# Kernel tuning notes

Measured on AMD Instinct MI355X. Metric: run time of the kernel, lower is better.

## Reference

```python
import jax, jax.numpy as jnp
import numpy as np

B, S, D = 2, 2048, 1024
FC = 4096
H = 16
EPS = 1e-5


def _layer_norm(x, g, b):
    mu = jnp.mean(x, axis=-1, keepdims=True)
    var = jnp.var(x, axis=-1, keepdims=True)
    return (x - mu) * jax.lax.rsqrt(var + EPS) * g + b


def setup_inputs() -> dict:
    key = jax.random.key(0)
    ks = jax.random.split(key, 8)
    s = 0.02
    return {
        "x": jax.random.normal(ks[0], (B, S, D), dtype=jnp.float32),
        "ln1_g": jnp.ones((D,), jnp.float32),
        "ln1_b": jnp.zeros((D,), jnp.float32),
        "w_qkv": jax.random.normal(ks[1], (D, 3 * D), dtype=jnp.float32) * s,
        "b_qkv": jnp.zeros((3 * D,), jnp.float32),
        "ln2_g": jnp.ones((D,), jnp.float32),
        "ln2_b": jnp.zeros((D,), jnp.float32),
        "w1": jax.random.normal(ks[2], (D, FC), dtype=jnp.float32) * s,
        "b1": jnp.zeros((FC,), jnp.float32),
        "w2": jax.random.normal(ks[3], (FC, D), dtype=jnp.float32) * s,
        "b2": jnp.zeros((D,), jnp.float32),
    }


def reference(x, ln1_g, ln1_b, w_qkv, b_qkv, ln2_g, ln2_b, w1, b1, w2, b2):
    # pre-LN attention block
    h = _layer_norm(x, ln1_g, ln1_b)
    qkv = h @ w_qkv + b_qkv                       # [B,S,3D]
    q, k, v = jnp.split(qkv, 3, axis=-1)
    hd = D // H
    q = q.reshape(B, S, H, hd)
    k = k.reshape(B, S, H, hd)
    v = v.reshape(B, S, H, hd)
    scale = 1.0 / jnp.sqrt(jnp.float32(hd))
    scores = jnp.einsum("bqhd,bkhd->bhqk", q, k) * scale
    a = jax.nn.softmax(scores, axis=-1)           # [B,H,S,S]
    attn = jnp.einsum("bhqk,bkhd->bqhd", a, v).reshape(B, S, D)
    attn = attn + x
    # MLP block
    h2 = _layer_norm(attn, ln2_g, ln2_b)
    m = jax.nn.relu(h2 @ w1 + b1)
    out = m @ w2 + b2 + attn
    return out
```

## Files before the change

### kernel.cpp

```cpp
#include <hip/hip_runtime.h>
#include <stdint.h>

typedef __bf16 bf16x8 __attribute__((ext_vector_type(8)));
typedef __bf16 bf16x4 __attribute__((ext_vector_type(4)));
typedef float f32x4 __attribute__((ext_vector_type(4)));

__device__ __forceinline__ void g2l16(const void* gp, void* lp) {
  __builtin_amdgcn_global_load_lds(
      (__attribute__((address_space(1))) void*)const_cast<void*>(gp),
      (__attribute__((address_space(3))) void*)lp, 16, 0, 0);
}

__global__ __launch_bounds__(256) void ln_bf16(
    const float* __restrict__ in, const float* __restrict__ g,
    const float* __restrict__ b, __bf16* __restrict__ out) {
  int row = blockIdx.x;
  int t = threadIdx.x;
  const float4* rp = (const float4*)(in + (size_t)row * 1024);
  float4 v = rp[t];
  float s = v.x + v.y + v.z + v.w;
  float ss = v.x * v.x + v.y * v.y + v.z * v.z + v.w * v.w;
#pragma unroll
  for (int o = 32; o; o >>= 1) {
    s += __shfl_down(s, o, 64);
    ss += __shfl_down(ss, o, 64);
  }
  __shared__ float red[8];
  int w = t >> 6;
  if ((t & 63) == 0) { red[w] = s; red[4 + w] = ss; }
  __syncthreads();
  float S1 = red[0] + red[1] + red[2] + red[3];
  float S2 = red[4] + red[5] + red[6] + red[7];
  float mu = S1 * (1.0f / 1024.0f);
  float var = S2 * (1.0f / 1024.0f) - mu * mu;
  float rstd = rsqrtf(var + 1e-5f);
  int c = t * 4;
  float4 gv = ((const float4*)g)[t];
  float4 bv = ((const float4*)b)[t];
  __bf16* op = out + (size_t)row * 1024 + c;
  op[0] = (__bf16)((v.x - mu) * rstd * gv.x + bv.x);
  op[1] = (__bf16)((v.y - mu) * rstd * gv.y + bv.y);
  op[2] = (__bf16)((v.z - mu) * rstd * gv.z + bv.z);
  op[3] = (__bf16)((v.w - mu) * rstd * gv.w + bv.w);
}

__global__ __launch_bounds__(256) void tcast(const float* __restrict__ in,
                                             __bf16* __restrict__ out, int R,
                                             int C) {
  __shared__ float t[32][33];
  int c0 = blockIdx.x * 32, r0 = blockIdx.y * 32;
  int tx = threadIdx.x & 31, ty = threadIdx.x >> 5;
#pragma unroll
  for (int i = 0; i < 4; i++)
    t[ty + i * 8][tx] = in[(size_t)(r0 + ty + i * 8) * C + c0 + tx];
  __syncthreads();
#pragma unroll
  for (int i = 0; i < 4; i++)
    out[(size_t)(c0 + ty + i * 8) * R + r0 + tx] = (__bf16)t[tx][ty + i * 8];
}

__global__ __launch_bounds__(256) void vtrans(const __bf16* __restrict__ qkv,
                                              __bf16* __restrict__ vT) {
  __shared__ __bf16 t[64][72];
  int bh = blockIdx.y, s0 = blockIdx.x * 64;
  int tid = threadIdx.x;
  int b = bh >> 4, h = bh & 15;
  int r = tid >> 2, c = (tid & 3) * 16;
  const __bf16* src =
      qkv + (size_t)(b * 2048 + s0 + r) * 3072 + 2048 + h * 64 + c;
  *(bf16x8*)&t[r][c] = *(const bf16x8*)src;
  *(bf16x8*)&t[r][c + 8] = *(const bf16x8*)(src + 8);
  __syncthreads();
  int d = tid >> 2;
  int cs = (tid & 3) * 16;
  __bf16 tmp[16] __attribute__((aligned(16)));
#pragma unroll
  for (int u = 0; u < 16; u++) tmp[u] = t[cs + u][d];
  __bf16* dst = vT + (size_t)(bh * 64 + d) * 2048 + s0 + cs;
  *(bf16x8*)dst = *(bf16x8*)&tmp[0];
  *(bf16x8*)(dst + 8) = *(bf16x8*)&tmp[8];
}

template <int EPI>
__global__ __launch_bounds__(256) void gemm_bt(
    const __bf16* __restrict__ A, const __bf16* __restrict__ BT,
    const float* __restrict__ bias, const float* __restrict__ res,
    void* __restrict__ out, int M, int N, int K) {
  __shared__ __bf16 As[128 * 32];
  __shared__ __bf16 Bs[128 * 32];
  int tid = threadIdx.x;
  int m0 = blockIdx.y * 128, n0 = blockIdx.x * 128;
  int lane = tid & 63, w = tid >> 6;
  int wm = (w >> 1) * 64, wn = (w & 1) * 64;
  int quad = lane >> 4, lm = lane & 15;

  int kc = K / (int)gridDim.z;
  int kBeg = (int)blockIdx.z * kc;
  int kEnd = kBeg + kc;

  f32x4 acc[4][4] = {};

  int sr = tid >> 2;
  int sc = (((tid & 3) - ((tid >> 3) & 3)) & 3) * 8;
  const __bf16* aRow = A + (size_t)(m0 + sr) * K + sc;
  const __bf16* bRow = BT + (size_t)(n0 + sr) * K + sc;
  size_t step64a = (size_t)64 * K;

  for (int k0 = kBeg; k0 < kEnd; k0 += 32) {
    g2l16(aRow + k0, &As[tid * 8]);
    g2l16(aRow + step64a + k0, &As[2048 + tid * 8]);
    g2l16(bRow + k0, &Bs[tid * 8]);
    g2l16(bRow + step64a + k0, &Bs[2048 + tid * 8]);
    __syncthreads();
    bf16x8 af[4], bv[4];
#pragma unroll
    for (int i = 0; i < 4; i++) {
      int ar = wm + i * 16 + lm;
      af[i] = *(const bf16x8*)&As[ar * 32 + ((quad + (ar >> 1)) & 3) * 8];
    }
#pragma unroll
    for (int j = 0; j < 4; j++) {
      int br = wn + j * 16 + lm;
      bv[j] = *(const bf16x8*)&Bs[br * 32 + ((quad + (br >> 1)) & 3) * 8];
    }
#pragma unroll
    for (int i = 0; i < 4; i++)
#pragma unroll
      for (int j = 0; j < 4; j++)
        acc[i][j] =
            __builtin_amdgcn_mfma_f32_16x16x32_bf16(af[i], bv[j], acc[i][j], 0, 0, 0);
    __syncthreads();
  }

#pragma unroll
  for (int i = 0; i < 4; i++)
#pragma unroll
    for (int j = 0; j < 4; j++) {
      int rg0 = m0 + wm + i * 16 + quad * 4;
      int cg = n0 + wn + j * 16 + lm;
      float bi = (EPI == 3) ? 0.0f : bias[cg];
#pragma unroll
      for (int r = 0; r < 4; r++) {
        int rg = rg0 + r;
        float v = acc[i][j][r] + bi;
        if (EPI == 1) v = fmaxf(v, 0.0f);
        if (EPI == 2) {
          ((float*)out)[(size_t)rg * N + cg] = v + res[(size_t)rg * N + cg];
        } else if (EPI == 3) {
          ((__bf16*)out)[(size_t)blockIdx.z * M * N + (size_t)rg * N + cg] =
              (__bf16)v;
        } else {
          ((__bf16*)out)[(size_t)rg * N + cg] = (__bf16)v;
        }
      }
    }
}

__global__ __launch_bounds__(256) void reduce_mlp2(
    const __bf16* __restrict__ part, const float* __restrict__ bias,
    const float* __restrict__ res, float* __restrict__ out) {
  size_t i = ((size_t)blockIdx.x * 256 + threadIdx.x) * 8;
  const size_t plane = (size_t)4096 * 1024;
  bf16x8 p0 = *(const bf16x8*)(part + i);
  bf16x8 p1 = *(const bf16x8*)(part + plane + i);
  bf16x8 p2 = *(const bf16x8*)(part + 2 * plane + i);
  bf16x8 p3 = *(const bf16x8*)(part + 3 * plane + i);
  int n0 = (int)(i & 1023);
  float4 b0 = *(const float4*)(bias + n0);
  float4 b1 = *(const float4*)(bias + n0 + 4);
  float4 r0 = *(const float4*)(res + i);
  float4 r1 = *(const float4*)(res + i + 4);
  float4 o0, o1;
  o0.x = (float)p0[0] + (float)p1[0] + (float)p2[0] + (float)p3[0] + b0.x + r0.x;
  o0.y = (float)p0[1] + (float)p1[1] + (float)p2[1] + (float)p3[1] + b0.y + r0.y;
  o0.z = (float)p0[2] + (float)p1[2] + (float)p2[2] + (float)p3[2] + b0.z + r0.z;
  o0.w = (float)p0[3] + (float)p1[3] + (float)p2[3] + (float)p3[3] + b0.w + r0.w;
  o1.x = (float)p0[4] + (float)p1[4] + (float)p2[4] + (float)p3[4] + b1.x + r1.x;
  o1.y = (float)p0[5] + (float)p1[5] + (float)p2[5] + (float)p3[5] + b1.y + r1.y;
  o1.z = (float)p0[6] + (float)p1[6] + (float)p2[6] + (float)p3[6] + b1.z + r1.z;
  o1.w = (float)p0[7] + (float)p1[7] + (float)p2[7] + (float)p3[7] + b1.w + r1.w;
  *(float4*)(out + i) = o0;
  *(float4*)(out + i + 4) = o1;
}

__global__ __launch_bounds__(512) void attn_kernel(
    const __bf16* __restrict__ qkv, const __bf16* __restrict__ vT,
    const float* __restrict__ x, float* __restrict__ attnres) {
  int qb = blockIdx.x, h = blockIdx.y, b = blockIdx.z;
  int tid = threadIdx.x, lane = tid & 63, w = tid >> 6;
  int quad = lane >> 4, lm = lane & 15;
  int q0 = qb * 128;

  __shared__ __bf16 Qs[128 * 64];
  __shared__ __bf16 Kbuf[2][64 * 64];
  __shared__ __bf16 Vbuf[3][64 * 64];
  __shared__ __bf16 Ps[8][16 * 72];

  const __bf16* qbase = qkv + (size_t)(b * 2048) * 3072 + h * 64;
  const __bf16* kbase = qkv + (size_t)(b * 2048) * 3072 + 1024 + h * 64;
  const __bf16* vbase = vT + (size_t)((b * 16 + h) * 64) * 2048;

  int sr = tid >> 3;
  int sc = (((tid & 7) - sr) & 7) * 8;

  g2l16(qbase + (size_t)(q0 + sr) * 3072 + sc, &Qs[tid * 8]);
  g2l16(qbase + (size_t)(q0 + 64 + sr) * 3072 + sc, &Qs[4096 + tid * 8]);
  g2l16(kbase + (size_t)sr * 3072 + sc, &Kbuf[0][tid * 8]);
  g2l16(vbase + (size_t)sr * 2048 + sc, &Vbuf[0][tid * 8]);
  __syncthreads();

  int qrow = w * 16 + lm;
  bf16x8 qf0 = *(const bf16x8*)&Qs[qrow * 64 + ((quad + qrow) & 7) * 8];
  bf16x8 qf1 = *(const bf16x8*)&Qs[qrow * 64 + ((4 + quad + qrow) & 7) * 8];

  f32x4 acc_o[4] = {};
  float rs = 0.0f;
  const float cexp = 0.18033688f;

  const __bf16* kpre = kbase + (size_t)(64 + sr) * 3072 + sc;
  const __bf16* vpre = vbase + (size_t)sr * 2048 + 64 + sc;
  __bf16* pv = Vbuf[2];
  __bf16* cv = Vbuf[0];
  __bf16* nv = Vbuf[1];
  int kcur = 0;

  for (int t = 0; t < 32; ++t) {
    bf16x8 pf0 = *(const bf16x8*)&Ps[w][lm * 72 + quad * 8];
    bf16x8 pf1 = *(const bf16x8*)&Ps[w][lm * 72 + 32 + quad * 8];
    if (t < 31) {
      g2l16(kpre, &Kbuf[kcur ^ 1][tid * 8]);
      g2l16(vpre, &nv[tid * 8]);
      kpre += (size_t)64 * 3072;
      vpre += 64;
    }
    const __bf16* Ks = Kbuf[kcur];
#pragma unroll
    for (int j = 0; j < 4; j++) {
      int krow = j * 16 + lm;
      bf16x8 kf0 = *(const bf16x8*)&Ks[krow * 64 + ((quad + krow) & 7) * 8];
      bf16x8 kf1 = *(const bf16x8*)&Ks[krow * 64 + ((4 + quad + krow) & 7) * 8];
      f32x4 z = {0.0f, 0.0f, 0.0f, 0.0f};
      z = __builtin_amdgcn_mfma_f32_16x16x32_bf16(kf0, qf0, z, 0, 0, 0);
      z = __builtin_amdgcn_mfma_f32_16x16x32_bf16(kf1, qf1, z, 0, 0, 0);
      bf16x4 pw;
#pragma unroll
      for (int rr = 0; rr < 4; rr++) {
        float e = exp2f(z[rr] * cexp);
        rs += e;
        pw[rr] = (__bf16)e;
      }
      *(bf16x4*)&Ps[w][lm * 72 + j * 16 + quad * 4] = pw;
    }
    if (t > 0) {
#pragma unroll
      for (int jd = 0; jd < 4; jd++) {
        int vrow = jd * 16 + lm;
        bf16x8 vf0 = *(const bf16x8*)&pv[vrow * 64 + ((quad + vrow) & 7) * 8];
        bf16x8 vf1 =
            *(const bf16x8*)&pv[vrow * 64 + ((4 + quad + vrow) & 7) * 8];
        acc_o[jd] = __builtin_amdgcn_mfma_f32_16x16x32_bf16(vf0, pf0,
                                                            acc_o[jd], 0, 0, 0);
        acc_o[jd] = __builtin_amdgcn_mfma_f32_16x16x32_bf16(vf1, pf1,
                                                            acc_o[jd], 0, 0, 0);
      }
    }
    __bf16* tmp = pv; pv = cv; cv = nv; nv = tmp;
    kcur ^= 1;
    __syncthreads();
  }

  {
    bf16x8 pf0 = *(const bf16x8*)&Ps[w][lm * 72 + quad * 8];
    bf16x8 pf1 = *(const bf16x8*)&Ps[w][lm * 72 + 32 + quad * 8];
#pragma unroll
    for (int jd = 0; jd < 4; jd++) {
      int vrow = jd * 16 + lm;
      bf16x8 vf0 = *(const bf16x8*)&pv[vrow * 64 + ((quad + vrow) & 7) * 8];
      bf16x8 vf1 = *(const bf16x8*)&pv[vrow * 64 + ((4 + quad + vrow) & 7) * 8];
      acc_o[jd] = __builtin_amdgcn_mfma_f32_16x16x32_bf16(vf0, pf0, acc_o[jd],
                                                          0, 0, 0);
      acc_o[jd] = __builtin_amdgcn_mfma_f32_16x16x32_bf16(vf1, pf1, acc_o[jd],
                                                          0, 0, 0);
    }
  }

  rs += __shfl_xor(rs, 16);
  rs += __shfl_xor(rs, 32);
  float inv = 1.0f / rs;

  int qg = q0 + w * 16 + lm;
  const float* xrow = x + ((size_t)(b * 2048 + qg)) * 1024 + h * 64;
  float* orow = attnres + ((size_t)(b * 2048 + qg)) * 1024 + h * 64;
#pragma unroll
  for (int jd = 0; jd < 4; jd++) {
    int d0 = jd * 16 + quad * 4;
    float4 xv = *(const float4*)(xrow + d0);
    float4 ov;
    ov.x = acc_o[jd][0] * inv + xv.x;
    ov.y = acc_o[jd][1] * inv + xv.y;
    ov.z = acc_o[jd][2] * inv + xv.z;
    ov.w = acc_o[jd][3] * inv + xv.w;
    *(float4*)(orow + d0) = ov;
  }
}

extern "C" void kernel_launch(void* const* d_in, const int* in_sizes, int n_in,
                              void* d_out, int out_size, void* d_ws,
                              size_t ws_size, hipStream_t stream) {
  const float* x = (const float*)d_in[0];
  const float* ln1_g = (const float*)d_in[1];
  const float* ln1_b = (const float*)d_in[2];
  const float* w_qkv = (const float*)d_in[3];
  const float* b_qkv = (const float*)d_in[4];
  const float* ln2_g = (const float*)d_in[5];
  const float* ln2_b = (const float*)d_in[6];
  const float* w1 = (const float*)d_in[7];
  const float* b1 = (const float*)d_in[8];
  const float* w2 = (const float*)d_in[9];
  const float* b2 = (const float*)d_in[10];
  float* out = (float*)d_out;

  char* ws = (char*)d_ws;
  size_t o = 0;
  float* attnres = (float*)(ws + o);  o += (size_t)4096 * 1024 * 4;
  __bf16* mmid = (__bf16*)(ws + o);   o += (size_t)4096 * 4096 * 2;
  __bf16* w2T = (__bf16*)(ws + o);    o += (size_t)1024 * 4096 * 2;
  size_t base2 = o;
  __bf16* h1 = (__bf16*)(ws + o);     o += (size_t)4096 * 1024 * 2;
  __bf16* wqkvT = (__bf16*)(ws + o);  o += (size_t)3072 * 1024 * 2;
  __bf16* w1T = (__bf16*)(ws + o);    o += (size_t)4096 * 1024 * 2;
  __bf16* qkvb = (__bf16*)(ws + o);   o += (size_t)4096 * 3072 * 2;
  __bf16* vTb = (__bf16*)(ws + o);    o += (size_t)32 * 64 * 2048 * 2;
  __bf16* h2 = (__bf16*)(ws + o);     o += (size_t)4096 * 1024 * 2;
  __bf16* partials = (__bf16*)(ws + base2);

  tcast<<<dim3(96, 32), 256, 0, stream>>>(w_qkv, wqkvT, 1024, 3072);
  tcast<<<dim3(128, 32), 256, 0, stream>>>(w1, w1T, 1024, 4096);
  tcast<<<dim3(32, 128), 256, 0, stream>>>(w2, w2T, 4096, 1024);

  ln_bf16<<<4096, 256, 0, stream>>>(x, ln1_g, ln1_b, h1);
  gemm_bt<0><<<dim3(24, 32), 256, 0, stream>>>(h1, wqkvT, b_qkv, nullptr, qkvb,
                                               4096, 3072, 1024);
  vtrans<<<dim3(32, 32), 256, 0, stream>>>(qkvb, vTb);
  attn_kernel<<<dim3(16, 16, 2), 512, 0, stream>>>(qkvb, vTb, x, attnres);
  ln_bf16<<<4096, 256, 0, stream>>>(attnres, ln2_g, ln2_b, h2);
  gemm_bt<1><<<dim3(32, 32), 256, 0, stream>>>(h2, w1T, b1, nullptr, mmid, 4096,
                                               4096, 1024);
  gemm_bt<3><<<dim3(8, 32, 4), 256, 0, stream>>>(mmid, w2T, nullptr, nullptr,
                                                 partials, 4096, 1024, 4096);
  reduce_mlp2<<<2048, 256, 0, stream>>>(partials, b2, attnres, out);
}
```

Before: 362.6 us.

## Give each attention wave two 16-row query tiles to reuse K/V fragments

The attention kernel drops from 8 waves to 4 waves per block, and each wave now handles 32 query rows as two 16-row tiles. Every K and V fragment read from LDS feeds two MFMAs instead of one, which halves LDS fragment traffic per unit of compute. The global-to-LDS loads are split into two halves to fit 256 threads. The cost is more registers per wave (two sets of accumulators and Q fragments), fewer waves to hide latency, and more load instructions per thread.

```diff
diff --git a/kernel.cpp b/kernel.cpp
--- a/kernel.cpp
+++ b/kernel.cpp
@@ -183,7 +183,7 @@
   *(float4*)(out + i + 4) = o1;
 }
 
-__global__ __launch_bounds__(512) void attn_kernel(
+__global__ __launch_bounds__(256) void attn_kernel(
     const __bf16* __restrict__ qkv, const __bf16* __restrict__ vT,
     const float* __restrict__ x, float* __restrict__ attnres) {
   int qb = blockIdx.x, h = blockIdx.y, b = blockIdx.z;
@@ -194,7 +194,7 @@
   __shared__ __bf16 Qs[128 * 64];
   __shared__ __bf16 Kbuf[2][64 * 64];
   __shared__ __bf16 Vbuf[3][64 * 64];
-  __shared__ __bf16 Ps[8][16 * 72];
+  __shared__ __bf16 Ps[4][32 * 72];
 
   const __bf16* qbase = qkv + (size_t)(b * 2048) * 3072 + h * 64;
   const __bf16* kbase = qkv + (size_t)(b * 2048) * 3072 + 1024 + h * 64;
@@ -203,18 +203,28 @@
   int sr = tid >> 3;
   int sc = (((tid & 7) - sr) & 7) * 8;
 
-  g2l16(qbase + (size_t)(q0 + sr) * 3072 + sc, &Qs[tid * 8]);
-  g2l16(qbase + (size_t)(q0 + 64 + sr) * 3072 + sc, &Qs[4096 + tid * 8]);
+#pragma unroll
+  for (int i = 0; i < 4; i++)
+    g2l16(qbase + (size_t)(q0 + i * 32 + sr) * 3072 + sc,
+          &Qs[i * 2048 + tid * 8]);
   g2l16(kbase + (size_t)sr * 3072 + sc, &Kbuf[0][tid * 8]);
+  g2l16(kbase + (size_t)(32 + sr) * 3072 + sc, &Kbuf[0][2048 + tid * 8]);
   g2l16(vbase + (size_t)sr * 2048 + sc, &Vbuf[0][tid * 8]);
+  g2l16(vbase + (size_t)(32 + sr) * 2048 + sc, &Vbuf[0][2048 + tid * 8]);
   __syncthreads();
 
-  int qrow = w * 16 + lm;
-  bf16x8 qf0 = *(const bf16x8*)&Qs[qrow * 64 + ((quad + qrow) & 7) * 8];
-  bf16x8 qf1 = *(const bf16x8*)&Qs[qrow * 64 + ((4 + quad + qrow) & 7) * 8];
-
-  f32x4 acc_o[4] = {};
-  float rs = 0.0f;
+  bf16x8 qf[2][2];
+#pragma unroll
+  for (int i = 0; i < 2; i++) {
+    int qrow = w * 32 + i * 16 + lm;
+#pragma unroll
+    for (int kk = 0; kk < 2; kk++)
+      qf[i][kk] =
+          *(const bf16x8*)&Qs[qrow * 64 + ((kk * 4 + quad + qrow) & 7) * 8];
+  }
+
+  f32x4 acc_o[2][4] = {};
+  float rs[2] = {0.0f, 0.0f};
   const float cexp = 0.18033688f;
 
   const __bf16* kpre = kbase + (size_t)(64 + sr) * 3072 + sc;
@@ -225,11 +235,17 @@
   int kcur = 0;
 
   for (int t = 0; t < 32; ++t) {
-    bf16x8 pf0 = *(const bf16x8*)&Ps[w][lm * 72 + quad * 8];
-    bf16x8 pf1 = *(const bf16x8*)&Ps[w][lm * 72 + 32 + quad * 8];
+    bf16x8 pf[2][2];
+#pragma unroll
+    for (int i = 0; i < 2; i++) {
+      pf[i][0] = *(const bf16x8*)&Ps[w][(i * 16 + lm) * 72 + quad * 8];
+      pf[i][1] = *(const bf16x8*)&Ps[w][(i * 16 + lm) * 72 + 32 + quad * 8];
+    }
     if (t < 31) {
       g2l16(kpre, &Kbuf[kcur ^ 1][tid * 8]);
+      g2l16(kpre + (size_t)32 * 3072, &Kbuf[kcur ^ 1][2048 + tid * 8]);
       g2l16(vpre, &nv[tid * 8]);
+      g2l16(vpre + (size_t)32 * 2048, &nv[2048 + tid * 8]);
       kpre += (size_t)64 * 3072;
       vpre += 64;
     }
@@ -239,17 +255,20 @@
       int krow = j * 16 + lm;
       bf16x8 kf0 = *(const bf16x8*)&Ks[krow * 64 + ((quad + krow) & 7) * 8];
       bf16x8 kf1 = *(const bf16x8*)&Ks[krow * 64 + ((4 + quad + krow) & 7) * 8];
-      f32x4 z = {0.0f, 0.0f, 0.0f, 0.0f};
-      z = __builtin_amdgcn_mfma_f32_16x16x32_bf16(kf0, qf0, z, 0, 0, 0);
-      z = __builtin_amdgcn_mfma_f32_16x16x32_bf16(kf1, qf1, z, 0, 0, 0);
-      bf16x4 pw;
-#pragma unroll
-      for (int rr = 0; rr < 4; rr++) {
-        float e = exp2f(z[rr] * cexp);
-        rs += e;
-        pw[rr] = (__bf16)e;
+#pragma unroll
+      for (int i = 0; i < 2; i++) {
+        f32x4 z = {0.0f, 0.0f, 0.0f, 0.0f};
+        z = __builtin_amdgcn_mfma_f32_16x16x32_bf16(kf0, qf[i][0], z, 0, 0, 0);
+        z = __builtin_amdgcn_mfma_f32_16x16x32_bf16(kf1, qf[i][1], z, 0, 0, 0);
+        bf16x4 pw;
+#pragma unroll
+        for (int rr = 0; rr < 4; rr++) {
+          float e = exp2f(z[rr] * cexp);
+          rs[i] += e;
+          pw[rr] = (__bf16)e;
+        }
+        *(bf16x4*)&Ps[w][(i * 16 + lm) * 72 + j * 16 + quad * 4] = pw;
       }
-      *(bf16x4*)&Ps[w][lm * 72 + j * 16 + quad * 4] = pw;
     }
     if (t > 0) {
 #pragma unroll
@@ -258,10 +277,13 @@
         bf16x8 vf0 = *(const bf16x8*)&pv[vrow * 64 + ((quad + vrow) & 7) * 8];
         bf16x8 vf1 =
             *(const bf16x8*)&pv[vrow * 64 + ((4 + quad + vrow) & 7) * 8];
-        acc_o[jd] = __builtin_amdgcn_mfma_f32_16x16x32_bf16(vf0, pf0,
-                                                            acc_o[jd], 0, 0, 0);
-        acc_o[jd] = __builtin_amdgcn_mfma_f32_16x16x32_bf16(vf1, pf1,
-                                                            acc_o[jd], 0, 0, 0);
+#pragma unroll
+        for (int i = 0; i < 2; i++) {
+          acc_o[i][jd] = __builtin_amdgcn_mfma_f32_16x16x32_bf16(
+              vf0, pf[i][0], acc_o[i][jd], 0, 0, 0);
+          acc_o[i][jd] = __builtin_amdgcn_mfma_f32_16x16x32_bf16(
+              vf1, pf[i][1], acc_o[i][jd], 0, 0, 0);
+        }
       }
     }
     __bf16* tmp = pv; pv = cv; cv = nv; nv = tmp;
@@ -270,37 +292,47 @@
   }
 
   {
-    bf16x8 pf0 = *(const bf16x8*)&Ps[w][lm * 72 + quad * 8];
-    bf16x8 pf1 = *(const bf16x8*)&Ps[w][lm * 72 + 32 + quad * 8];
+    bf16x8 pf[2][2];
+#pragma unroll
+    for (int i = 0; i < 2; i++) {
+      pf[i][0] = *(const bf16x8*)&Ps[w][(i * 16 + lm) * 72 + quad * 8];
+      pf[i][1] = *(const bf16x8*)&Ps[w][(i * 16 + lm) * 72 + 32 + quad * 8];
+    }
 #pragma unroll
     for (int jd = 0; jd < 4; jd++) {
       int vrow = jd * 16 + lm;
       bf16x8 vf0 = *(const bf16x8*)&pv[vrow * 64 + ((quad + vrow) & 7) * 8];
       bf16x8 vf1 = *(const bf16x8*)&pv[vrow * 64 + ((4 + quad + vrow) & 7) * 8];
-      acc_o[jd] = __builtin_amdgcn_mfma_f32_16x16x32_bf16(vf0, pf0, acc_o[jd],
-                                                          0, 0, 0);
-      acc_o[jd] = __builtin_amdgcn_mfma_f32_16x16x32_bf16(vf1, pf1, acc_o[jd],
-                                                          0, 0, 0);
-    }
-  }
-
-  rs += __shfl_xor(rs, 16);
-  rs += __shfl_xor(rs, 32);
-  float inv = 1.0f / rs;
-
-  int qg = q0 + w * 16 + lm;
-  const float* xrow = x + ((size_t)(b * 2048 + qg)) * 1024 + h * 64;
-  float* orow = attnres + ((size_t)(b * 2048 + qg)) * 1024 + h * 64;
-#pragma unroll
-  for (int jd = 0; jd < 4; jd++) {
-    int d0 = jd * 16 + quad * 4;
-    float4 xv = *(const float4*)(xrow + d0);
-    float4 ov;
-    ov.x = acc_o[jd][0] * inv + xv.x;
-    ov.y = acc_o[jd][1] * inv + xv.y;
-    ov.z = acc_o[jd][2] * inv + xv.z;
-    ov.w = acc_o[jd][3] * inv + xv.w;
-    *(float4*)(orow + d0) = ov;
+#pragma unroll
+      for (int i = 0; i < 2; i++) {
+        acc_o[i][jd] = __builtin_amdgcn_mfma_f32_16x16x32_bf16(
+            vf0, pf[i][0], acc_o[i][jd], 0, 0, 0);
+        acc_o[i][jd] = __builtin_amdgcn_mfma_f32_16x16x32_bf16(
+            vf1, pf[i][1], acc_o[i][jd], 0, 0, 0);
+      }
+    }
+  }
+
+#pragma unroll
+  for (int i = 0; i < 2; i++) {
+    float v = rs[i];
+    v += __shfl_xor(v, 16);
+    v += __shfl_xor(v, 32);
+    float inv = 1.0f / v;
+    int qg = q0 + w * 32 + i * 16 + lm;
+    const float* xrow = x + ((size_t)(b * 2048 + qg)) * 1024 + h * 64;
+    float* orow = attnres + ((size_t)(b * 2048 + qg)) * 1024 + h * 64;
+#pragma unroll
+    for (int jd = 0; jd < 4; jd++) {
+      int d0 = jd * 16 + quad * 4;
+      float4 xv = *(const float4*)(xrow + d0);
+      float4 ov;
+      ov.x = acc_o[i][jd][0] * inv + xv.x;
+      ov.y = acc_o[i][jd][1] * inv + xv.y;
+      ov.z = acc_o[i][jd][2] * inv + xv.z;
+      ov.w = acc_o[i][jd][3] * inv + xv.w;
+      *(float4*)(orow + d0) = ov;
+    }
   }
 }
 
@@ -342,7 +374,7 @@
   gemm_bt<0><<<dim3(24, 32), 256, 0, stream>>>(h1, wqkvT, b_qkv, nullptr, qkvb,
                                                4096, 3072, 1024);
   vtrans<<<dim3(32, 32), 256, 0, stream>>>(qkvb, vTb);
-  attn_kernel<<<dim3(16, 16, 2), 512, 0, stream>>>(qkvb, vTb, x, attnres);
+  attn_kernel<<<dim3(16, 16, 2), 256, 0, stream>>>(qkvb, vTb, x, attnres);
   ln_bf16<<<4096, 256, 0, stream>>>(attnres, ln2_g, ln2_b, h2);
   gemm_bt<1><<<dim3(32, 32), 256, 0, stream>>>(h2, w1T, b1, nullptr, mmid, 4096,
                                                4096, 1024);
```

Result: slower. 372.5 us (+2.7%).
